# Optimization experiments

Hardware: AMD Instinct MI355X
Metric: run time of the kernel (lower is better)

The kernel has to match this reference:

```python
import jax, jax.numpy as jnp
import numpy as np

MODEL_DIM = 128
NUM_HEADS = 8

def setup_inputs() -> dict:
    key = jax.random.key(0)
    kx, kq, kk, kv = jax.random.split(key, 4)
    B, S, D, H = 4, 2048, MODEL_DIM, NUM_HEADS
    scale = 1.0 / np.sqrt(D)
    x = jax.random.normal(kx, (B, S, D), dtype=jnp.float32)
    # nn.Linear weights: shape [out_features, in_features] = [H*D, D]
    W_q = jax.random.normal(kq, (H * D, D), dtype=jnp.float32) * scale
    W_k = jax.random.normal(kk, (H * D, D), dtype=jnp.float32) * scale
    W_v = jax.random.normal(kv, (H * D, D), dtype=jnp.float32) * scale
    return {"x": x, "W_q": W_q, "W_k": W_k, "W_v": W_v}

def reference(x, W_q, W_k, W_v):
    B, S, D = x.shape
    H = NUM_HEADS
    # projections: y = x @ W.T, then split heads -> [B, H, S, D]
    def proj(W):
        y = jnp.einsum('bsd,ed->bse', x, W)  # [B, S, H*D]
        return y.reshape(B, S, H, D).transpose(0, 2, 1, 3)
    Q, K, V = proj(W_q), proj(W_k), proj(W_v)
    # scores [B, H, S, S]
    A = jnp.einsum('bhsd,bhtd->bhst', Q, K) / jnp.sqrt(jnp.asarray(D, x.dtype))
    # AV then softmax over the model_dim axis (as in original: softmax after matmul)
    Z = jax.nn.softmax(jnp.einsum('bhst,bhtd->bhsd', A, V), axis=-1)
    return Z
```

## Files before the change

### kernel.cpp

```cpp
#include <hip/hip_runtime.h>
#include <hip/hip_bf16.h>


#define NB 4
#define NS 2048
#define ND 128
#define NH 8
#define EPB (NS * ND)
#define XFRAGS (512 * 4)
#define WFRAGS (3 * 64 * 4)
#define PS_ELEMS ((size_t)2 * XFRAGS * 512 + (size_t)2 * WFRAGS * 512)

typedef unsigned short u16;
typedef unsigned int u32;
typedef short bf16x8 __attribute__((ext_vector_type(8)));
typedef float f32x4 __attribute__((ext_vector_type(4)));

struct __align__(16) us8 { u16 u[8]; };

#define MFMA(a, b, c) __builtin_amdgcn_mfma_f32_16x16x32_bf16((a), (b), (c), 0, 0, 0)

__device__ __forceinline__ void splitf(float f, u16& hi, u16& lo) {
    u32 fb = __float_as_uint(f);
    u32 hb = fb + 0x7FFFu + ((fb >> 16) & 1u);
    hi = (u16)(hb >> 16);
    float fh = __uint_as_float((hb >> 16) << 16);
    float fl = f - fh;
    u32 lb = __float_as_uint(fl);
    u32 lr = lb + 0x7FFFu + ((lb >> 16) & 1u);
    lo = (u16)(lr >> 16);
}

__global__ __launch_bounds__(256) void presplit_kernel(
    const float* __restrict__ xg, const float* __restrict__ Wqg,
    const float* __restrict__ Wkg, const float* __restrict__ Wvg,
    u16* __restrict__ ps)
{
    const int gid = blockIdx.x * 256 + threadIdx.x;
    const int total = (XFRAGS + WFRAGS) * 64;
    if (gid >= total) return;
    const int fi = gid >> 6, l = gid & 63;
    const float* src;
    u16 *H, *L;
    if (fi < XFRAGS) {
        const int m16 = fi >> 2, kc = fi & 3;
        src = xg + (size_t)(m16 * 16 + (l & 15)) * ND + kc * 32 + (l >> 4) * 8;
        H = ps + (size_t)fi * 512 + l * 8;
        L = H + (size_t)XFRAGS * 512;
    } else {
        const int wfi = fi - XFRAGS;
        const int e16g = wfi >> 2, kc = wfi & 3;
        const int t = e16g >> 6, e16 = e16g & 63;
        const float* Wt = (t == 0) ? Wqg : (t == 1) ? Wkg : Wvg;
        src = Wt + (size_t)(e16 * 16 + (l & 15)) * ND + kc * 32 + (l >> 4) * 8;
        H = ps + (size_t)2 * XFRAGS * 512 + (size_t)wfi * 512 + l * 8;
        L = H + (size_t)WFRAGS * 512;
    }
    float4 v0 = *(const float4*)src;
    float4 v1 = *(const float4*)(src + 4);
    float vv[8] = { v0.x, v0.y, v0.z, v0.w, v1.x, v1.y, v1.z, v1.w };
    us8 hh, ll;
    #pragma unroll
    for (int j = 0; j < 8; ++j) splitf(vv[j], hh.u[j], ll.u[j]);
    *(us8*)H = hh;
    *(us8*)L = ll;
}

__global__ __launch_bounds__(256) void proj_kernel(
    const u16* __restrict__ ps, u16* __restrict__ ws, int b0, int nbh)
{
    __shared__ u32 sE[8192];

    const int which = blockIdx.z;
    const int tid = threadIdx.x;
    const int wv = tid >> 6;
    const int l  = tid & 63;
    const int c  = l & 15;
    const int g  = l >> 4;
    const int wr = wv & 1;
    const int wc = wv >> 1;
    const int bx = blockIdx.x;
    const int bgl = bx >> 5;
    const int slb = (bx & 31) * 64;
    const int h = blockIdx.y;
    const int m0 = (b0 + bgl) * NS + slb;

    const u16* XH = ps;
    const u16* XL = ps + (size_t)XFRAGS * 512;
    const u16* WH = ps + (size_t)2 * XFRAGS * 512;
    const u16* WL = WH + (size_t)WFRAGS * 512;

    const int m16b = (m0 >> 4) + wr * 2;
    bf16x8 ah[2][4], al[2][4];
    #pragma unroll
    for (int mi = 0; mi < 2; ++mi)
        #pragma unroll
        for (int kc = 0; kc < 4; ++kc) {
            size_t f = ((size_t)(m16b + mi) * 4 + kc) * 512 + l * 8;
            ah[mi][kc] = *(const bf16x8*)(XH + f);
            al[mi][kc] = *(const bf16x8*)(XL + f);
        }

    f32x4 acc[2][4];
    #pragma unroll
    for (int mi = 0; mi < 2; ++mi)
        #pragma unroll
        for (int ni = 0; ni < 4; ++ni) acc[mi][ni] = (f32x4){0.f, 0.f, 0.f, 0.f};

    const int e16b = which * 64 + h * 8 + wc * 4;
    #pragma unroll
    for (int kc = 0; kc < 4; ++kc) {
        bf16x8 bh[4], bl[4];
        #pragma unroll
        for (int ni = 0; ni < 4; ++ni) {
            size_t f = ((size_t)(e16b + ni) * 4 + kc) * 512 + l * 8;
            bh[ni] = *(const bf16x8*)(WH + f);
            bl[ni] = *(const bf16x8*)(WL + f);
        }
        #pragma unroll
        for (int mi = 0; mi < 2; ++mi)
            #pragma unroll
            for (int ni = 0; ni < 4; ++ni) {
                acc[mi][ni] = MFMA(ah[mi][kc], bh[ni], acc[mi][ni]);
                acc[mi][ni] = MFMA(ah[mi][kc], bl[ni], acc[mi][ni]);
                acc[mi][ni] = MFMA(al[mi][kc], bh[ni], acc[mi][ni]);
            }
    }

    #pragma unroll
    for (int mi = 0; mi < 2; ++mi)
        #pragma unroll
        for (int ni = 0; ni < 4; ++ni)
            #pragma unroll
            for (int r = 0; r < 4; ++r) {
                const int slL = wr * 32 + mi * 16 + 4 * g + r;
                const int d   = wc * 64 + ni * 16 + c;
                u16 ph, pl;
                splitf(acc[mi][ni][r], ph, pl);
                u32 off;
                if (which == 0)
                    off = (u32)(((slL >> 4) * 4 + (d >> 5)) * 512
                          + ((d >> 3) & 3) * 128 + (slL & 15) * 8 + (d & 7));
                else if (which == 1)
                    off = (u32)(((((slL >> 5) * 4 + (d >> 5)) * 2 + ((slL >> 4) & 1)) * 512)
                          + ((d >> 3) & 3) * 128 + (slL & 15) * 8 + (d & 7));
                else
                    off = (u32)(((slL >> 5) * 8 + (d >> 4)) * 512
                          + ((slL >> 3) & 3) * 128 + (d & 15) * 8 + (slL & 7));
                sE[off] = (u32)ph | ((u32)pl << 16);
            }
    __syncthreads();

    const size_t TS = (size_t)nbh * EPB;
    const size_t tb = (size_t)(bgl * NH + h) * EPB;
    u16* HB = ws + (size_t)(2 * which) * TS + tb + (size_t)slb * 128;
    u16* LB = HB + TS;
    #pragma unroll
    for (int c4 = 0; c4 < 4; ++c4) {
        const int idx = c4 * 2048 + tid * 8;
        us8 hh, ll;
        #pragma unroll
        for (int j = 0; j < 8; ++j) {
            u32 v = sE[idx + j];
            hh.u[j] = (u16)(v & 0xFFFFu);
            ll.u[j] = (u16)(v >> 16);
        }
        *(us8*)(HB + idx) = hh;
        *(us8*)(LB + idx) = ll;
    }
}

__global__ __launch_bounds__(256, 2) void attn_kernel(
    const u16* __restrict__ ws, float* __restrict__ outg, int b0, int nbh)
{
    __shared__ __align__(16) u16 sbuf[2][4][4096];
    __shared__ u32 sP[4][32 * 17];

    const int tid = threadIdx.x;
    const int Wv = tid >> 6;
    const int l  = tid & 63;
    const int c  = l & 15;
    const int g  = l >> 4;
    const int bhl = blockIdx.y;
    const size_t tb = (size_t)bhl * EPB;
    const size_t TS = (size_t)nbh * EPB;

    const u16* QH = ws;
    const u16* QL = ws + 1 * TS;
    const u16* KH = ws + 2 * TS;
    const u16* KL = ws + 3 * TS;
    const u16* VH = ws + 4 * TS;
    const u16* VL = ws + 5 * TS;

    const int qb = blockIdx.x * 128 + Wv * 32;

    bf16x8 qh[2][4], ql[2][4];
    #pragma unroll
    for (int mi = 0; mi < 2; ++mi)
        #pragma unroll
        for (int kc = 0; kc < 4; ++kc) {
            size_t f = tb + ((size_t)(((qb + 16 * mi) >> 4) * 4 + kc) * 64 + l) * 8;
            qh[mi][kc] = *(const bf16x8*)(QH + f);
            ql[mi][kc] = *(const bf16x8*)(QL + f);
        }

    f32x4 z[2][8];
    #pragma unroll
    for (int mi = 0; mi < 2; ++mi)
        #pragma unroll
        for (int ni = 0; ni < 8; ++ni) z[mi][ni] = (f32x4){0.f, 0.f, 0.f, 0.f};

    const u16* srcs[4] = { KH, KL, VH, VL };
    auto stage = [&](int buf, int T) {
        #pragma unroll
        for (int t4 = 0; t4 < 4; ++t4)
            #pragma unroll
            for (int r = 0; r < 2; ++r)
                __builtin_amdgcn_global_load_lds(
                    (const __attribute__((address_space(1))) void*)
                        (srcs[t4] + tb + (size_t)T * 4096 + r * 2048 + tid * 8),
                    (__attribute__((address_space(3))) void*)
                        (&sbuf[buf][t4][r * 2048 + tid * 8]),
                    16, 0, 0);
    };

    u32* sPW = &sP[Wv][0];
    const float scale = 0.08838834764831845f;

    stage(0, 0);

    for (int T = 0; T < 64; ++T) {
        const int cur = T & 1;
        if (T < 63) {
            stage(cur ^ 1, T + 1);
            asm volatile("s_waitcnt vmcnt(8)" ::: "memory");
        } else {
            asm volatile("s_waitcnt vmcnt(0)" ::: "memory");
        }
        __builtin_amdgcn_s_barrier();
        asm volatile("" ::: "memory");

        const u16* bKH = &sbuf[cur][0][0];
        const u16* bKL = &sbuf[cur][1][0];
        const u16* bVH = &sbuf[cur][2][0];
        const u16* bVL = &sbuf[cur][3][0];

        f32x4 s[2][2];
        #pragma unroll
        for (int mi = 0; mi < 2; ++mi)
            #pragma unroll
            for (int nt = 0; nt < 2; ++nt) s[mi][nt] = (f32x4){0.f, 0.f, 0.f, 0.f};
        __builtin_amdgcn_s_setprio(1);
        #pragma unroll
        for (int kc = 0; kc < 4; ++kc) {
            bf16x8 kh0 = *(const bf16x8*)(bKH + ((kc * 2 + 0) * 64 + l) * 8);
            bf16x8 kh1 = *(const bf16x8*)(bKH + ((kc * 2 + 1) * 64 + l) * 8);
            bf16x8 kl0 = *(const bf16x8*)(bKL + ((kc * 2 + 0) * 64 + l) * 8);
            bf16x8 kl1 = *(const bf16x8*)(bKL + ((kc * 2 + 1) * 64 + l) * 8);
            #pragma unroll
            for (int mi = 0; mi < 2; ++mi) {
                s[mi][0] = MFMA(qh[mi][kc], kh0, s[mi][0]);
                s[mi][0] = MFMA(qh[mi][kc], kl0, s[mi][0]);
                s[mi][0] = MFMA(ql[mi][kc], kh0, s[mi][0]);
                s[mi][1] = MFMA(qh[mi][kc], kh1, s[mi][1]);
                s[mi][1] = MFMA(qh[mi][kc], kl1, s[mi][1]);
                s[mi][1] = MFMA(ql[mi][kc], kh1, s[mi][1]);
            }
        }
        __builtin_amdgcn_s_setprio(0);

        bf16x8 pa_h[2], pa_l[2];
        #pragma unroll
        for (int mi = 0; mi < 2; ++mi) {
            #pragma unroll
            for (int nt = 0; nt < 2; ++nt)
                #pragma unroll
                for (int r = 0; r < 4; ++r) {
                    float p = s[mi][nt][r] * scale;
                    u16 ph, pl; splitf(p, ph, pl);
                    sPW[(nt * 16 + c) * 17 + 4 * g + r] = (u32)ph | ((u32)pl << 16);
                }
            union { u16 uh[8]; bf16x8 v; } ph8;
            union { u16 ul[8]; bf16x8 v; } pl8;
            #pragma unroll
            for (int j = 0; j < 8; ++j) {
                u32 v = sPW[(8 * g + j) * 17 + c];
                ph8.uh[j] = (u16)(v & 0xFFFFu);
                pl8.ul[j] = (u16)(v >> 16);
            }
            pa_h[mi] = ph8.v;
            pa_l[mi] = pl8.v;
        }

        __builtin_amdgcn_s_setprio(1);
        #pragma unroll
        for (int ni = 0; ni < 8; ++ni) {
            bf16x8 vh = *(const bf16x8*)(bVH + (ni * 64 + l) * 8);
            bf16x8 vl = *(const bf16x8*)(bVL + (ni * 64 + l) * 8);
            #pragma unroll
            for (int mi = 0; mi < 2; ++mi) {
                z[mi][ni] = MFMA(pa_h[mi], vh, z[mi][ni]);
                z[mi][ni] = MFMA(pa_h[mi], vl, z[mi][ni]);
                z[mi][ni] = MFMA(pa_l[mi], vh, z[mi][ni]);
            }
        }
        __builtin_amdgcn_s_setprio(0);

        asm volatile("" ::: "memory");
        __builtin_amdgcn_s_barrier();
    }

    const size_t obase = (size_t)(b0 * NH + bhl) * EPB;
    #pragma unroll
    for (int mi = 0; mi < 2; ++mi)
        #pragma unroll
        for (int r = 0; r < 4; ++r) {
            float v[8];
            float m = -3.4e38f;
            #pragma unroll
            for (int ni = 0; ni < 8; ++ni) { v[ni] = z[mi][ni][r]; m = fmaxf(m, v[ni]); }
            #pragma unroll
            for (int off = 1; off < 16; off <<= 1) m = fmaxf(m, __shfl_xor(m, off, 64));
            float sum = 0.f;
            #pragma unroll
            for (int ni = 0; ni < 8; ++ni) { v[ni] = expf(v[ni] - m); sum += v[ni]; }
            #pragma unroll
            for (int off = 1; off < 16; off <<= 1) sum += __shfl_xor(sum, off, 64);
            const float inv = 1.f / sum;
            const int q = qb + 16 * mi + 4 * g + r;
            #pragma unroll
            for (int ni = 0; ni < 8; ++ni)
                outg[obase + (size_t)q * ND + ni * 16 + c] = v[ni] * inv;
        }
}

extern "C" void kernel_launch(void* const* d_in, const int* in_sizes, int n_in,
                              void* d_out, int out_size, void* d_ws, size_t ws_size,
                              hipStream_t stream)
{
    (void)out_size;
    int xi = 0;
    for (int i = 0; i < n_in && i < 4; ++i)
        if (in_sizes[i] == NB * NS * ND) { xi = i; break; }
    const float* x = (const float*)d_in[xi];
    const float* Wsp[3]; int w = 0;
    for (int i = 0; i < 4; ++i) if (i != xi) Wsp[w++] = (const float*)d_in[i];
    const float* Wq = Wsp[0];
    const float* Wk = Wsp[1];
    const float* Wv = Wsp[2];
    float* out = (float*)d_out;
    u16* ws = (u16*)d_ws;

    auto need_bytes = [](int nb) {
        return ((size_t)6 * nb * NH * EPB + PS_ELEMS) * 2;
    };
    int nb = (ws_size >= need_bytes(4)) ? 4 : (ws_size >= need_bytes(2)) ? 2 : 1;
    const int nbh = nb * NH;
    u16* psb = ws + (size_t)6 * nbh * EPB;

    {
        const int total = (XFRAGS + WFRAGS) * 64;
        presplit_kernel<<<dim3((total + 255) / 256), dim3(256), 0, stream>>>(
            x, Wq, Wk, Wv, psb);
    }

    for (int b0 = 0; b0 < NB; b0 += nb) {
        proj_kernel<<<dim3(nb * 32, 8, 3), dim3(256), 0, stream>>>(
            psb, ws, b0, nbh);
        attn_kernel<<<dim3(16, nbh), dim3(256), 0, stream>>>(
            ws, out, b0, nbh);
    }
}
```

Measured before the change: 296.7 us.

## Single-buffer K/V staging and shrink P scratch to raise occupancy to four blocks

Replaces the double-buffered K/V LDS staging with a single buffer and halves the per-wave P transpose scratch by processing the two key sub-tiles in turn. Launch bounds go from 2 to 4 blocks per CU so more waves can hide latency. The cost is losing the overlap of global loads with compute: each iteration now waits for its full load between two barriers. Tighter register limits may also cause spills.

```diff
diff --git a/kernel.cpp b/kernel.cpp
--- a/kernel.cpp
+++ b/kernel.cpp
@@ -170,11 +170,11 @@
     }
 }
 
-__global__ __launch_bounds__(256, 2) void attn_kernel(
+__global__ __launch_bounds__(256, 4) void attn_kernel(
     const u16* __restrict__ ws, float* __restrict__ outg, int b0, int nbh)
 {
-    __shared__ __align__(16) u16 sbuf[2][4][4096];
-    __shared__ u32 sP[4][32 * 17];
+    __shared__ __align__(16) u16 sbuf[4][4096];
+    __shared__ u32 sP[4][16 * 17];
 
     const int tid = threadIdx.x;
     const int Wv = tid >> 6;
@@ -211,7 +211,7 @@
         for (int ni = 0; ni < 8; ++ni) z[mi][ni] = (f32x4){0.f, 0.f, 0.f, 0.f};
 
     const u16* srcs[4] = { KH, KL, VH, VL };
-    auto stage = [&](int buf, int T) {
+    auto stage = [&](int T) {
         #pragma unroll
         for (int t4 = 0; t4 < 4; ++t4)
             #pragma unroll
@@ -220,31 +220,23 @@
                     (const __attribute__((address_space(1))) void*)
                         (srcs[t4] + tb + (size_t)T * 4096 + r * 2048 + tid * 8),
                     (__attribute__((address_space(3))) void*)
-                        (&sbuf[buf][t4][r * 2048 + tid * 8]),
+                        (&sbuf[t4][r * 2048 + tid * 8]),
                     16, 0, 0);
     };
 
     u32* sPW = &sP[Wv][0];
     const float scale = 0.08838834764831845f;
 
-    stage(0, 0);
+    stage(0);
+    asm volatile("s_waitcnt vmcnt(0)" ::: "memory");
+    __builtin_amdgcn_s_barrier();
+
+    const u16* bKH = &sbuf[0][0];
+    const u16* bKL = &sbuf[1][0];
+    const u16* bVH = &sbuf[2][0];
+    const u16* bVL = &sbuf[3][0];
 
     for (int T = 0; T < 64; ++T) {
-        const int cur = T & 1;
-        if (T < 63) {
-            stage(cur ^ 1, T + 1);
-            asm volatile("s_waitcnt vmcnt(8)" ::: "memory");
-        } else {
-            asm volatile("s_waitcnt vmcnt(0)" ::: "memory");
-        }
-        __builtin_amdgcn_s_barrier();
-        asm volatile("" ::: "memory");
-
-        const u16* bKH = &sbuf[cur][0][0];
-        const u16* bKL = &sbuf[cur][1][0];
-        const u16* bVH = &sbuf[cur][2][0];
-        const u16* bVL = &sbuf[cur][3][0];
-
         f32x4 s[2][2];
         #pragma unroll
         for (int mi = 0; mi < 2; ++mi)
@@ -272,21 +264,29 @@
         bf16x8 pa_h[2], pa_l[2];
         #pragma unroll
         for (int mi = 0; mi < 2; ++mi) {
-            #pragma unroll
-            for (int nt = 0; nt < 2; ++nt)
+            u32 got[8];
+            #pragma unroll
+            for (int nt = 0; nt < 2; ++nt) {
                 #pragma unroll
                 for (int r = 0; r < 4; ++r) {
                     float p = s[mi][nt][r] * scale;
                     u16 ph, pl; splitf(p, ph, pl);
-                    sPW[(nt * 16 + c) * 17 + 4 * g + r] = (u32)ph | ((u32)pl << 16);
+                    sPW[c * 17 + 4 * g + r] = (u32)ph | ((u32)pl << 16);
                 }
+                asm volatile("s_waitcnt lgkmcnt(0)" ::: "memory");
+                if ((g >> 1) == nt) {
+                    #pragma unroll
+                    for (int j = 0; j < 8; ++j)
+                        got[j] = sPW[(8 * (g & 1) + j) * 17 + c];
+                }
+                asm volatile("s_waitcnt lgkmcnt(0)" ::: "memory");
+            }
             union { u16 uh[8]; bf16x8 v; } ph8;
             union { u16 ul[8]; bf16x8 v; } pl8;
             #pragma unroll
             for (int j = 0; j < 8; ++j) {
-                u32 v = sPW[(8 * g + j) * 17 + c];
-                ph8.uh[j] = (u16)(v & 0xFFFFu);
-                pl8.ul[j] = (u16)(v >> 16);
+                ph8.uh[j] = (u16)(got[j] & 0xFFFFu);
+                pl8.ul[j] = (u16)(got[j] >> 16);
             }
             pa_h[mi] = ph8.v;
             pa_l[mi] = pl8.v;
@@ -307,6 +307,9 @@
         __builtin_amdgcn_s_setprio(0);
 
         asm volatile("" ::: "memory");
+        __builtin_amdgcn_s_barrier();
+        if (T < 63) stage(T + 1);
+        asm volatile("s_waitcnt vmcnt(0)" ::: "memory");
         __builtin_amdgcn_s_barrier();
     }
 
```

Measured after the change: 683.0 us. 130% more time.
